# Kernel optimization log

Measured on AMD Instinct MI355X. Metric: run time of the kernel, lower is better.

## Reference

```python
import jax, jax.numpy as jnp
import numpy as np
import math

NUM_HEADS = 8
HEAD_DIM = 16  # hidden_features 128 / 8 heads
SCALE = 1.0 / math.sqrt(HEAD_DIM)


def setup_inputs() -> dict:
    key = jax.random.key(0)
    ks = jax.random.split(key, 9)
    N, E, F = 50000, 640000, 128
    node_h = jax.random.normal(ks[0], (N, F), jnp.float32)
    edge_h = jax.random.normal(ks[1], (E, F), jnp.float32)
    # distances kept strictly positive so distance**lambda (and its grad) is well-defined
    distance = jax.random.uniform(ks[2], (E, 1), jnp.float32, minval=0.1, maxval=1.0)
    src = jax.random.randint(ks[3], (E,), 0, N, jnp.int32)
    dst = jax.random.randint(ks[4], (E,), 0, N, jnp.int32)

    def lin(k):
        kw, kb = jax.random.split(k)
        W = jax.random.normal(kw, (F, F), jnp.float32) / math.sqrt(F)
        b = jax.random.normal(kb, (F,), jnp.float32) * 0.02
        return W, b

    Wq, bq = lin(ks[5])
    Wk, bk = lin(ks[6])
    Wv, bv = lin(ks[7])
    Wo, bo = lin(ks[8])
    lam = jnp.array(1.0, jnp.float32)  # attenuation_lambda (clamp in original is a no-op)
    return dict(node_h=node_h, edge_h=edge_h, distance=distance,
                Wq=Wq, bq=bq, Wk=Wk, bk=bk, Wv=Wv, bv=bv, Wo=Wo, bo=bo,
                lam=lam, src=src, dst=dst)


def _segment_softmax(logits, seg, num):
    # softmax over edges sharing the same destination node (DGL mailbox dim=1)
    m = jax.ops.segment_max(logits, seg, num_segments=num)
    m = jax.lax.stop_gradient(jnp.where(jnp.isfinite(m), m, 0.0))
    e = jnp.exp(logits - m[seg])
    den = jax.ops.segment_sum(e, seg, num_segments=num)
    den = jnp.where(den == 0, 1.0, den)  # guard zero in-degree nodes
    return e / den[seg]


def reference(node_h, edge_h, distance, Wq, bq, Wk, bk, Wv, bv, Wo, bo, lam, src, dst):
    N = node_h.shape[0]
    q = (node_h @ Wq.T + bq).reshape(N, NUM_HEADS, HEAD_DIM)
    k = (edge_h @ Wk.T + bk).reshape(-1, NUM_HEADS, HEAD_DIM)
    v = (node_h @ Wv.T + bv).reshape(N, NUM_HEADS, HEAD_DIM)
    qs, qd = q[src], q[dst]                      # [E, H, d] gathers
    in_m = jnp.sum(qs * k, axis=-1)              # [E, H]
    out_m = jnp.sum(qd * k, axis=-1)             # [E, H]
    diag_m = jnp.sum(qs * qd, axis=-1)           # [E, H]
    att = jnp.power(distance, lam)               # [E, 1] power-law attenuation
    score = (_segment_softmax(in_m * SCALE, dst, N)
             + _segment_softmax(out_m * SCALE, dst, N)
             + _segment_softmax(diag_m * SCALE, dst, N)) * att  # [E, H]
    # message value is edges.dst['v'] (as in the original), scatter-sum to dst
    h = jax.ops.segment_sum(score[..., None] * v[dst], dst, num_segments=N)
    h = h.reshape(N, NUM_HEADS * HEAD_DIM)
    out = h @ Wo.T + bo
    return jax.nn.leaky_relu(out, negative_slope=0.1)  # dropout is identity in eval
```

## Files before the change

kernel.cpp:

```cpp
#include <hip/hip_runtime.h>
#include <math.h>

#define H 8
#define FD 128
#define SCALE 0.25f
#define EPB 128

typedef __attribute__((ext_vector_type(8))) short bf16x8;
typedef __attribute__((ext_vector_type(4))) float f32x4;

__device__ __forceinline__ unsigned short bf_rne(float f) {
    unsigned u = __float_as_uint(f);
    u += 0x7FFFu + ((u >> 16) & 1u);
    return (unsigned short)(u >> 16);
}
__device__ __forceinline__ float bf_to_f(unsigned short s) {
    return __uint_as_float(((unsigned)s) << 16);
}

__global__ __launch_bounds__(256) void edge_kernel(
    const float* __restrict__ eh, const float* __restrict__ Wk,
    const float* __restrict__ bk, const float* __restrict__ q,
    const int* __restrict__ src, const int* __restrict__ dst,
    float* __restrict__ l1, float* __restrict__ l2, float* __restrict__ l3,
    int E) {
    __shared__ unsigned short lW[128 * 128];
    __shared__ unsigned short lA[128 * 128];
    const int t = threadIdx.x;
    const int e0 = blockIdx.x * EPB;

#pragma unroll
    for (int i = 0; i < 16; ++i) {
        int flat = i * 256 + t;
        int row = flat >> 5;
        int c4 = flat & 31;
        float4 w = *(const float4*)(Wk + row * 128 + c4 * 4);
        int blk = (c4 >> 1) ^ (row & 7);
        ushort4 p = make_ushort4(bf_rne(w.x), bf_rne(w.y), bf_rne(w.z), bf_rne(w.w));
        *(ushort4*)(lW + row * 128 + blk * 8 + (c4 & 1) * 4) = p;
    }
#pragma unroll
    for (int i = 0; i < 16; ++i) {
        int flat = i * 256 + t;
        int row = flat >> 5;
        int c4 = flat & 31;
        int e = e0 + row;
        if (e >= E) e = E - 1;
        float4 w = *(const float4*)(eh + (size_t)e * 128 + c4 * 4);
        int blk = (c4 >> 1) ^ (row & 7);
        ushort4 p = make_ushort4(bf_rne(w.x), bf_rne(w.y), bf_rne(w.z), bf_rne(w.w));
        *(ushort4*)(lA + row * 128 + blk * 8 + (c4 & 1) * 4) = p;
    }
    __syncthreads();

    const int lane = t & 63;
    const int wv = t >> 6;
    const int lm = lane & 15;
    const int lq = lane >> 4;
    const int wm = wv * 32;

    bf16x8 a[2][4];
#pragma unroll
    for (int mt = 0; mt < 2; ++mt)
#pragma unroll
        for (int s = 0; s < 4; ++s) {
            int row = wm + mt * 16 + lm;
            int swb = (s * 4 + lq) ^ (row & 7);
            a[mt][s] = *(const bf16x8*)(lA + row * 128 + swb * 8);
        }

    f32x4 acc[2][8];
#pragma unroll
    for (int nt = 0; nt < 8; ++nt) {
        float b = bk[nt * 16 + lm];
#pragma unroll
        for (int mt = 0; mt < 2; ++mt) {
            acc[mt][nt][0] = b; acc[mt][nt][1] = b;
            acc[mt][nt][2] = b; acc[mt][nt][3] = b;
        }
    }
#pragma unroll
    for (int s = 0; s < 4; ++s) {
#pragma unroll
        for (int nt = 0; nt < 8; ++nt) {
            int row = nt * 16 + lm;
            int swb = (s * 4 + lq) ^ (row & 7);
            bf16x8 bf = *(const bf16x8*)(lW + row * 128 + swb * 8);
#pragma unroll
            for (int mt = 0; mt < 2; ++mt)
                acc[mt][nt] = __builtin_amdgcn_mfma_f32_16x16x32_bf16(
                    a[mt][s], bf, acc[mt][nt], 0, 0, 0);
        }
    }
    __syncthreads();
#pragma unroll
    for (int mt = 0; mt < 2; ++mt)
#pragma unroll
        for (int nt = 0; nt < 8; ++nt)
#pragma unroll
            for (int r = 0; r < 4; ++r) {
                int m = wm + mt * 16 + lq * 4 + r;
                int n = nt * 16 + lm;
                int swb = (n >> 3) ^ (m & 7);
                lA[m * 128 + swb * 8 + (n & 7)] = bf_rne(acc[mt][nt][r]);
            }
    __syncthreads();

#pragma unroll
    for (int i = 0; i < 4; ++i) {
        int p = i * 256 + t;
        int el = p >> 3, h = p & 7;
        int e = e0 + el;
        if (e >= E) continue;
        int si = src[e], di = dst[e];
        const float* qsp = q + (size_t)si * FD + h * 16;
        const float* qdp = q + (size_t)di * FD + h * 16;
        float4 s0 = *(const float4*)(qsp);
        float4 s1 = *(const float4*)(qsp + 4);
        float4 s2 = *(const float4*)(qsp + 8);
        float4 s3 = *(const float4*)(qsp + 12);
        float4 d0 = *(const float4*)(qdp);
        float4 d1 = *(const float4*)(qdp + 4);
        float4 d2 = *(const float4*)(qdp + 8);
        float4 d3 = *(const float4*)(qdp + 12);
        int swb0 = (2 * h) ^ (el & 7);
        int swb1 = (2 * h + 1) ^ (el & 7);
        bf16x8 k0 = *(const bf16x8*)(lA + el * 128 + swb0 * 8);
        bf16x8 k1 = *(const bf16x8*)(lA + el * 128 + swb1 * 8);
        float qsv[16] = { s0.x, s0.y, s0.z, s0.w, s1.x, s1.y, s1.z, s1.w,
                          s2.x, s2.y, s2.z, s2.w, s3.x, s3.y, s3.z, s3.w };
        float qdv[16] = { d0.x, d0.y, d0.z, d0.w, d1.x, d1.y, d1.z, d1.w,
                          d2.x, d2.y, d2.z, d2.w, d3.x, d3.y, d3.z, d3.w };
        float pin = 0.f, pot = 0.f, pdg = 0.f;
#pragma unroll
        for (int j = 0; j < 8; ++j) {
            float kf = bf_to_f((unsigned short)k0[j]);
            pin += qsv[j] * kf; pot += qdv[j] * kf; pdg += qsv[j] * qdv[j];
        }
#pragma unroll
        for (int j = 0; j < 8; ++j) {
            float kf = bf_to_f((unsigned short)k1[j]);
            pin += qsv[8 + j] * kf; pot += qdv[8 + j] * kf;
            pdg += qsv[8 + j] * qdv[8 + j];
        }
        size_t gi = (size_t)e * H + h;
        l1[gi] = pin * SCALE;
        l2[gi] = pot * SCALE;
        l3[gi] = pdg * SCALE;
    }
}

__global__ __launch_bounds__(256) void den_kernel(
    float* __restrict__ l1, float* __restrict__ l2, float* __restrict__ l3,
    const int* __restrict__ dst, const float* __restrict__ distance,
    const float* __restrict__ lam, float* __restrict__ den1,
    float* __restrict__ den2, float* __restrict__ den3,
    float* __restrict__ att, int EH) {
    int idx = blockIdx.x * 256 + threadIdx.x;
    if (idx >= EH) return;
    int e = idx >> 3, h = idx & 7;
    int nb = dst[e] * H + h;
    float x1 = __expf(l1[idx]); l1[idx] = x1; atomicAdd(den1 + nb, x1);
    float x2 = __expf(l2[idx]); l2[idx] = x2; atomicAdd(den2 + nb, x2);
    float x3 = __expf(l3[idx]); l3[idx] = x3; atomicAdd(den3 + nb, x3);
    if (h == 0) att[e] = __powf(distance[e], lam[0]);
}

__global__ __launch_bounds__(256) void recip_kernel(
    float* __restrict__ den1, float* __restrict__ den2,
    float* __restrict__ den3, int NH) {
    int idx = blockIdx.x * 256 + threadIdx.x;
    if (idx >= NH) return;
    float d1 = den1[idx]; den1[idx] = (d1 == 0.f) ? 0.f : 1.f / d1;
    float d2 = den2[idx]; den2[idx] = (d2 == 0.f) ? 0.f : 1.f / d2;
    float d3 = den3[idx]; den3[idx] = (d3 == 0.f) ? 0.f : 1.f / d3;
}

__global__ __launch_bounds__(256) void score_kernel(
    const float* __restrict__ l1, const float* __restrict__ l2,
    const float* __restrict__ l3, const float* __restrict__ den1,
    const float* __restrict__ den2, const float* __restrict__ den3,
    const int* __restrict__ dst, const float* __restrict__ att,
    float* __restrict__ ssum, int EH) {
    int idx = blockIdx.x * 256 + threadIdx.x;
    if (idx >= EH) return;
    int e = idx >> 3, h = idx & 7;
    int nb = dst[e] * H + h;
    float sc = (l1[idx] * den1[nb] + l2[idx] * den2[nb] + l3[idx] * den3[nb]) *
               att[e];
    atomicAdd(ssum + nb, sc);
}

__device__ __forceinline__ void load_w_lds(const float* __restrict__ W,
                                           float* Wl, int tid) {
    for (int x = tid; x < (FD * FD) / 4; x += 256) {
        int idx4 = x << 2;
        int i = idx4 >> 7;
        int j = idx4 & 127;
        float4 w = *(const float4*)(W + idx4);
        int col = (j + ((i >> 2) << 2)) & 127;
        *(float4*)(Wl + i * FD + col) = w;
    }
}

__global__ __launch_bounds__(256) void proj_kernel(
    const float* __restrict__ X, const float* __restrict__ W,
    const float* __restrict__ b, float* __restrict__ out, int Nrows) {
    __shared__ float Wl[FD * FD];
    int tid = threadIdx.x;
    load_w_lds(W, Wl, tid);
    __syncthreads();

    int fe = tid & 31;
    int te = tid >> 5;
    int row0 = blockIdx.x * 64;

    float4 bias = *(const float4*)(b + 4 * fe);
    float acc[8][4];
#pragma unroll
    for (int u = 0; u < 8; ++u) {
        acc[u][0] = bias.x; acc[u][1] = bias.y;
        acc[u][2] = bias.z; acc[u][3] = bias.w;
    }
    const float* Ar[8];
#pragma unroll
    for (int u = 0; u < 8; ++u) {
        int r = row0 + te + 8 * u;
        if (r >= Nrows) r = Nrows - 1;
        Ar[u] = X + (size_t)r * FD;
    }
    for (int j = 0; j < FD; j += 4) {
        int g = (j + 4 * fe) & 127;
        float4 w0 = *(float4*)(Wl + (4 * fe + 0) * FD + g);
        float4 w1 = *(float4*)(Wl + (4 * fe + 1) * FD + g);
        float4 w2 = *(float4*)(Wl + (4 * fe + 2) * FD + g);
        float4 w3 = *(float4*)(Wl + (4 * fe + 3) * FD + g);
#pragma unroll
        for (int u = 0; u < 8; ++u) {
            float4 a = *(const float4*)(Ar[u] + j);
            acc[u][0] += a.x * w0.x + a.y * w0.y + a.z * w0.z + a.w * w0.w;
            acc[u][1] += a.x * w1.x + a.y * w1.y + a.z * w1.z + a.w * w1.w;
            acc[u][2] += a.x * w2.x + a.y * w2.y + a.z * w2.z + a.w * w2.w;
            acc[u][3] += a.x * w3.x + a.y * w3.y + a.z * w3.z + a.w * w3.w;
        }
    }
#pragma unroll
    for (int u = 0; u < 8; ++u) {
        int r = row0 + te + 8 * u;
        if (r < Nrows) {
            float4 o;
            o.x = acc[u][0]; o.y = acc[u][1]; o.z = acc[u][2]; o.w = acc[u][3];
            *(float4*)(out + (size_t)r * FD + 4 * fe) = o;
        }
    }
}

__global__ __launch_bounds__(256) void out_kernel(
    const float* __restrict__ v, const float* __restrict__ ssum,
    const float* __restrict__ Wo, const float* __restrict__ bo,
    float* __restrict__ out, int Nrows) {
    __shared__ float Wl[FD * FD];
    int tid = threadIdx.x;
    load_w_lds(Wo, Wl, tid);
    __syncthreads();

    int fe = tid & 31;
    int te = tid >> 5;
    int row0 = blockIdx.x * 64;

    float4 bias = *(const float4*)(bo + 4 * fe);
    float acc[8][4];
#pragma unroll
    for (int u = 0; u < 8; ++u) {
        acc[u][0] = bias.x; acc[u][1] = bias.y;
        acc[u][2] = bias.z; acc[u][3] = bias.w;
    }
    int rv[8];
#pragma unroll
    for (int u = 0; u < 8; ++u) {
        int r = row0 + te + 8 * u;
        rv[u] = (r >= Nrows) ? (Nrows - 1) : r;
    }
    for (int j = 0; j < FD; j += 4) {
        int g = (j + 4 * fe) & 127;
        float4 w0 = *(float4*)(Wl + (4 * fe + 0) * FD + g);
        float4 w1 = *(float4*)(Wl + (4 * fe + 1) * FD + g);
        float4 w2 = *(float4*)(Wl + (4 * fe + 2) * FD + g);
        float4 w3 = *(float4*)(Wl + (4 * fe + 3) * FD + g);
        int hj = j >> 4;
#pragma unroll
        for (int u = 0; u < 8; ++u) {
            float4 a = *(const float4*)(v + (size_t)rv[u] * FD + j);
            float sc = ssum[rv[u] * H + hj];
            a.x *= sc; a.y *= sc; a.z *= sc; a.w *= sc;
            acc[u][0] += a.x * w0.x + a.y * w0.y + a.z * w0.z + a.w * w0.w;
            acc[u][1] += a.x * w1.x + a.y * w1.y + a.z * w1.z + a.w * w1.w;
            acc[u][2] += a.x * w2.x + a.y * w2.y + a.z * w2.z + a.w * w2.w;
            acc[u][3] += a.x * w3.x + a.y * w3.y + a.z * w3.z + a.w * w3.w;
        }
    }
#pragma unroll
    for (int u = 0; u < 8; ++u) {
        int r = row0 + te + 8 * u;
        if (r < Nrows) {
            float4 o;
            o.x = acc[u][0] > 0.f ? acc[u][0] : 0.1f * acc[u][0];
            o.y = acc[u][1] > 0.f ? acc[u][1] : 0.1f * acc[u][1];
            o.z = acc[u][2] > 0.f ? acc[u][2] : 0.1f * acc[u][2];
            o.w = acc[u][3] > 0.f ? acc[u][3] : 0.1f * acc[u][3];
            *(float4*)(out + (size_t)r * FD + 4 * fe) = o;
        }
    }
}

extern "C" void kernel_launch(void* const* d_in, const int* in_sizes, int n_in,
                              void* d_out, int out_size, void* d_ws,
                              size_t ws_size, hipStream_t stream) {
    (void)n_in; (void)out_size; (void)ws_size;
    const float* node_h   = (const float*)d_in[0];
    const float* edge_h   = (const float*)d_in[1];
    const float* distance = (const float*)d_in[2];
    const float* Wq = (const float*)d_in[3];
    const float* bq = (const float*)d_in[4];
    const float* Wk = (const float*)d_in[5];
    const float* bk = (const float*)d_in[6];
    const float* Wv = (const float*)d_in[7];
    const float* bv = (const float*)d_in[8];
    const float* Wo = (const float*)d_in[9];
    const float* bo = (const float*)d_in[10];
    const float* lam = (const float*)d_in[11];
    const int* src = (const int*)d_in[12];
    const int* dst = (const int*)d_in[13];

    int N = in_sizes[0] / FD;
    int E = in_sizes[1] / FD;

    char* ws = (char*)d_ws;
    float* q   = (float*)ws; ws += (size_t)N * FD * 4;
    float* v   = (float*)ws; ws += (size_t)N * FD * 4;
    float* l1  = (float*)ws; ws += (size_t)E * H * 4;
    float* l2  = (float*)ws; ws += (size_t)E * H * 4;
    float* l3  = (float*)ws; ws += (size_t)E * H * 4;
    float* att = (float*)ws; ws += (size_t)E * 4;
    char* zero_base = ws;
    float* den1 = (float*)ws; ws += (size_t)N * H * 4;
    float* den2 = (float*)ws; ws += (size_t)N * H * 4;
    float* den3 = (float*)ws; ws += (size_t)N * H * 4;
    float* ssum = (float*)ws; ws += (size_t)N * H * 4;

    hipMemsetAsync(zero_base, 0, (size_t)4 * N * H * 4, stream);

    int nb = (N + 63) / 64;
    proj_kernel<<<nb, 256, 0, stream>>>(node_h, Wq, bq, q, N);
    proj_kernel<<<nb, 256, 0, stream>>>(node_h, Wv, bv, v, N);

    int ebl = (E + EPB - 1) / EPB;
    edge_kernel<<<ebl, 256, 0, stream>>>(edge_h, Wk, bk, q, src, dst,
                                         l1, l2, l3, E);
    int EH = E * H;
    int sb = (EH + 255) / 256;
    den_kernel<<<sb, 256, 0, stream>>>(l1, l2, l3, dst, distance, lam,
                                       den1, den2, den3, att, EH);
    int NH = N * H;
    recip_kernel<<<(NH + 255) / 256, 256, 0, stream>>>(den1, den2, den3, NH);
    score_kernel<<<sb, 256, 0, stream>>>(l1, l2, l3, den1, den2, den3,
                                         dst, att, ssum, EH);
    out_kernel<<<nb, 256, 0, stream>>>(v, ssum, Wo, bo, (float*)d_out, N);
}
```

Measured before the change: 840.5 us.

## Fuse softmax passes into edge kernel and move projections to bf16 MFMA

Weights are pre-converted to bf16 once, and the Q/V projections are fused into one MFMA kernel that stores q in bf16. The edge kernel now exponentiates the logits directly and atomically accumulates both the softmax denominators and the attenuated numerators per destination node. This removes the E×H logit buffers and the separate den, recip and score passes. A small combine kernel divides the numerators by the denominators, and the output projection also uses bf16 MFMA. Skipping max subtraction in the softmax risks overflow for large logits, bf16 q and v lower precision, and the edge kernel now issues twice as many atomics.

```diff
diff --git a/kernel.cpp b/kernel.cpp
--- a/kernel.cpp
+++ b/kernel.cpp
@@ -4,7 +4,6 @@
 #define H 8
 #define FD 128
 #define SCALE 0.25f
-#define EPB 128
 
 typedef __attribute__((ext_vector_type(8))) short bf16x8;
 typedef __attribute__((ext_vector_type(4))) float f32x4;
@@ -17,58 +16,115 @@
 __device__ __forceinline__ float bf_to_f(unsigned short s) {
     return __uint_as_float(((unsigned)s) << 16);
 }
+__device__ __forceinline__ bf16x8 cvt8(const float* __restrict__ p) {
+    float4 a = *(const float4*)p;
+    float4 b = *(const float4*)(p + 4);
+    bf16x8 r;
+    r[0] = bf_rne(a.x); r[1] = bf_rne(a.y); r[2] = bf_rne(a.z); r[3] = bf_rne(a.w);
+    r[4] = bf_rne(b.x); r[5] = bf_rne(b.y); r[6] = bf_rne(b.z); r[7] = bf_rne(b.w);
+    return r;
+}
+
+__global__ __launch_bounds__(256) void prep_kernel(
+    const float* __restrict__ Wq, const float* __restrict__ Wk,
+    const float* __restrict__ Wv, const float* __restrict__ Wo,
+    unsigned short* __restrict__ oq, unsigned short* __restrict__ ok,
+    unsigned short* __restrict__ ov, unsigned short* __restrict__ oo) {
+    int i = blockIdx.x * 256 + threadIdx.x;
+    const float* src[4] = {Wq, Wk, Wv, Wo};
+    unsigned short* dstp[4] = {oq, ok, ov, oo};
+#pragma unroll
+    for (int m = 0; m < 4; ++m) {
+        float4 w = ((const float4*)src[m])[i];
+        ushort4 p = make_ushort4(bf_rne(w.x), bf_rne(w.y), bf_rne(w.z), bf_rne(w.w));
+        *(ushort4*)(dstp[m] + i * 4) = p;
+    }
+}
+
+__global__ __launch_bounds__(256) void qv_kernel(
+    const float* __restrict__ X, const unsigned short* __restrict__ Wqb,
+    const unsigned short* __restrict__ Wvb, const float* __restrict__ bq,
+    const float* __restrict__ bv, unsigned short* __restrict__ qb,
+    float* __restrict__ v, int Nrows) {
+    const int t = threadIdx.x;
+    const int lane = t & 63, wid = t >> 6;
+    const int lm = lane & 15, lq = lane >> 4;
+    const int r0 = blockIdx.x * 128 + wid * 32;
+
+    bf16x8 a[2][4];
+#pragma unroll
+    for (int mt = 0; mt < 2; ++mt)
+#pragma unroll
+        for (int s = 0; s < 4; ++s) {
+            int r = r0 + mt * 16 + lm;
+            if (r >= Nrows) r = Nrows - 1;
+            a[mt][s] = cvt8(X + (size_t)r * FD + s * 32 + lq * 8);
+        }
+#pragma unroll
+    for (int g = 0; g < 2; ++g) {
+        const unsigned short* Wb = g ? Wvb : Wqb;
+        const float* bias = g ? bv : bq;
+        f32x4 acc[2][8];
+#pragma unroll
+        for (int nt = 0; nt < 8; ++nt) {
+            float b = bias[nt * 16 + lm];
+#pragma unroll
+            for (int mt = 0; mt < 2; ++mt) {
+                acc[mt][nt][0] = b; acc[mt][nt][1] = b;
+                acc[mt][nt][2] = b; acc[mt][nt][3] = b;
+            }
+        }
+#pragma unroll
+        for (int s = 0; s < 4; ++s)
+#pragma unroll
+            for (int nt = 0; nt < 8; ++nt) {
+                bf16x8 bf = *(const bf16x8*)(Wb + (nt * 16 + lm) * FD + s * 32 + lq * 8);
+#pragma unroll
+                for (int mt = 0; mt < 2; ++mt)
+                    acc[mt][nt] = __builtin_amdgcn_mfma_f32_16x16x32_bf16(
+                        a[mt][s], bf, acc[mt][nt], 0, 0, 0);
+            }
+#pragma unroll
+        for (int mt = 0; mt < 2; ++mt)
+#pragma unroll
+            for (int nt = 0; nt < 8; ++nt)
+#pragma unroll
+                for (int r = 0; r < 4; ++r) {
+                    int row = r0 + mt * 16 + lq * 4 + r;
+                    if (row >= Nrows) continue;
+                    int col = nt * 16 + lm;
+                    if (g == 0)
+                        qb[(size_t)row * FD + col] = bf_rne(acc[mt][nt][r]);
+                    else
+                        v[(size_t)row * FD + col] = acc[mt][nt][r];
+                }
+    }
+}
 
 __global__ __launch_bounds__(256) void edge_kernel(
-    const float* __restrict__ eh, const float* __restrict__ Wk,
-    const float* __restrict__ bk, const float* __restrict__ q,
+    const float* __restrict__ eh, const unsigned short* __restrict__ Wkb,
+    const float* __restrict__ bk, const unsigned short* __restrict__ qb,
     const int* __restrict__ src, const int* __restrict__ dst,
-    float* __restrict__ l1, float* __restrict__ l2, float* __restrict__ l3,
-    int E) {
-    __shared__ unsigned short lW[128 * 128];
-    __shared__ unsigned short lA[128 * 128];
+    const float* __restrict__ distance, const float* __restrict__ lam,
+    float* __restrict__ den1, float* __restrict__ den2,
+    float* __restrict__ den3, float* __restrict__ sc1,
+    float* __restrict__ sc2, float* __restrict__ sc3, int E) {
+    __shared__ unsigned short lK[128 * 128];
     const int t = threadIdx.x;
-    const int e0 = blockIdx.x * EPB;
-
-#pragma unroll
-    for (int i = 0; i < 16; ++i) {
-        int flat = i * 256 + t;
-        int row = flat >> 5;
-        int c4 = flat & 31;
-        float4 w = *(const float4*)(Wk + row * 128 + c4 * 4);
-        int blk = (c4 >> 1) ^ (row & 7);
-        ushort4 p = make_ushort4(bf_rne(w.x), bf_rne(w.y), bf_rne(w.z), bf_rne(w.w));
-        *(ushort4*)(lW + row * 128 + blk * 8 + (c4 & 1) * 4) = p;
-    }
-#pragma unroll
-    for (int i = 0; i < 16; ++i) {
-        int flat = i * 256 + t;
-        int row = flat >> 5;
-        int c4 = flat & 31;
-        int e = e0 + row;
-        if (e >= E) e = E - 1;
-        float4 w = *(const float4*)(eh + (size_t)e * 128 + c4 * 4);
-        int blk = (c4 >> 1) ^ (row & 7);
-        ushort4 p = make_ushort4(bf_rne(w.x), bf_rne(w.y), bf_rne(w.z), bf_rne(w.w));
-        *(ushort4*)(lA + row * 128 + blk * 8 + (c4 & 1) * 4) = p;
-    }
-    __syncthreads();
-
-    const int lane = t & 63;
-    const int wv = t >> 6;
-    const int lm = lane & 15;
-    const int lq = lane >> 4;
-    const int wm = wv * 32;
+    const int e0 = blockIdx.x * 128;
+    const int lane = t & 63, wid = t >> 6;
+    const int lm = lane & 15, lq = lane >> 4;
+    const int wm = wid * 32;
 
     bf16x8 a[2][4];
 #pragma unroll
     for (int mt = 0; mt < 2; ++mt)
 #pragma unroll
         for (int s = 0; s < 4; ++s) {
-            int row = wm + mt * 16 + lm;
-            int swb = (s * 4 + lq) ^ (row & 7);
-            a[mt][s] = *(const bf16x8*)(lA + row * 128 + swb * 8);
-        }
-
+            int e = e0 + wm + mt * 16 + lm;
+            if (e >= E) e = E - 1;
+            a[mt][s] = cvt8(eh + (size_t)e * FD + s * 32 + lq * 8);
+        }
     f32x4 acc[2][8];
 #pragma unroll
     for (int nt = 0; nt < 8; ++nt) {
@@ -80,19 +136,15 @@
         }
     }
 #pragma unroll
-    for (int s = 0; s < 4; ++s) {
+    for (int s = 0; s < 4; ++s)
 #pragma unroll
         for (int nt = 0; nt < 8; ++nt) {
-            int row = nt * 16 + lm;
-            int swb = (s * 4 + lq) ^ (row & 7);
-            bf16x8 bf = *(const bf16x8*)(lW + row * 128 + swb * 8);
+            bf16x8 bf = *(const bf16x8*)(Wkb + (nt * 16 + lm) * FD + s * 32 + lq * 8);
 #pragma unroll
             for (int mt = 0; mt < 2; ++mt)
                 acc[mt][nt] = __builtin_amdgcn_mfma_f32_16x16x32_bf16(
                     a[mt][s], bf, acc[mt][nt], 0, 0, 0);
         }
-    }
-    __syncthreads();
 #pragma unroll
     for (int mt = 0; mt < 2; ++mt)
 #pragma unroll
@@ -102,10 +154,11 @@
                 int m = wm + mt * 16 + lq * 4 + r;
                 int n = nt * 16 + lm;
                 int swb = (n >> 3) ^ (m & 7);
-                lA[m * 128 + swb * 8 + (n & 7)] = bf_rne(acc[mt][nt][r]);
+                lK[m * 128 + swb * 8 + (n & 7)] = bf_rne(acc[mt][nt][r]);
             }
     __syncthreads();
 
+    const float lamv = lam[0];
 #pragma unroll
     for (int i = 0; i < 4; ++i) {
         int p = i * 256 + t;
@@ -113,204 +166,115 @@
         int e = e0 + el;
         if (e >= E) continue;
         int si = src[e], di = dst[e];
-        const float* qsp = q + (size_t)si * FD + h * 16;
-        const float* qdp = q + (size_t)di * FD + h * 16;
-        float4 s0 = *(const float4*)(qsp);
-        float4 s1 = *(const float4*)(qsp + 4);
-        float4 s2 = *(const float4*)(qsp + 8);
-        float4 s3 = *(const float4*)(qsp + 12);
-        float4 d0 = *(const float4*)(qdp);
-        float4 d1 = *(const float4*)(qdp + 4);
-        float4 d2 = *(const float4*)(qdp + 8);
-        float4 d3 = *(const float4*)(qdp + 12);
-        int swb0 = (2 * h) ^ (el & 7);
-        int swb1 = (2 * h + 1) ^ (el & 7);
-        bf16x8 k0 = *(const bf16x8*)(lA + el * 128 + swb0 * 8);
-        bf16x8 k1 = *(const bf16x8*)(lA + el * 128 + swb1 * 8);
-        float qsv[16] = { s0.x, s0.y, s0.z, s0.w, s1.x, s1.y, s1.z, s1.w,
-                          s2.x, s2.y, s2.z, s2.w, s3.x, s3.y, s3.z, s3.w };
-        float qdv[16] = { d0.x, d0.y, d0.z, d0.w, d1.x, d1.y, d1.z, d1.w,
-                          d2.x, d2.y, d2.z, d2.w, d3.x, d3.y, d3.z, d3.w };
+        const unsigned short* qsp = qb + (size_t)si * FD + h * 16;
+        const unsigned short* qdp = qb + (size_t)di * FD + h * 16;
+        bf16x8 qs0 = *(const bf16x8*)qsp;
+        bf16x8 qs1 = *(const bf16x8*)(qsp + 8);
+        bf16x8 qd0 = *(const bf16x8*)qdp;
+        bf16x8 qd1 = *(const bf16x8*)(qdp + 8);
+        int swb0 = (2 * h) ^ (el & 7), swb1 = (2 * h + 1) ^ (el & 7);
+        bf16x8 k0 = *(const bf16x8*)(lK + el * 128 + swb0 * 8);
+        bf16x8 k1 = *(const bf16x8*)(lK + el * 128 + swb1 * 8);
         float pin = 0.f, pot = 0.f, pdg = 0.f;
 #pragma unroll
         for (int j = 0; j < 8; ++j) {
+            float qsf = bf_to_f((unsigned short)qs0[j]);
+            float qdf = bf_to_f((unsigned short)qd0[j]);
             float kf = bf_to_f((unsigned short)k0[j]);
-            pin += qsv[j] * kf; pot += qdv[j] * kf; pdg += qsv[j] * qdv[j];
+            pin += qsf * kf; pot += qdf * kf; pdg += qsf * qdf;
         }
 #pragma unroll
         for (int j = 0; j < 8; ++j) {
+            float qsf = bf_to_f((unsigned short)qs1[j]);
+            float qdf = bf_to_f((unsigned short)qd1[j]);
             float kf = bf_to_f((unsigned short)k1[j]);
-            pin += qsv[8 + j] * kf; pot += qdv[8 + j] * kf;
-            pdg += qsv[8 + j] * qdv[8 + j];
-        }
-        size_t gi = (size_t)e * H + h;
-        l1[gi] = pin * SCALE;
-        l2[gi] = pot * SCALE;
-        l3[gi] = pdg * SCALE;
-    }
-}
-
-__global__ __launch_bounds__(256) void den_kernel(
-    float* __restrict__ l1, float* __restrict__ l2, float* __restrict__ l3,
-    const int* __restrict__ dst, const float* __restrict__ distance,
-    const float* __restrict__ lam, float* __restrict__ den1,
-    float* __restrict__ den2, float* __restrict__ den3,
-    float* __restrict__ att, int EH) {
-    int idx = blockIdx.x * 256 + threadIdx.x;
-    if (idx >= EH) return;
-    int e = idx >> 3, h = idx & 7;
-    int nb = dst[e] * H + h;
-    float x1 = __expf(l1[idx]); l1[idx] = x1; atomicAdd(den1 + nb, x1);
-    float x2 = __expf(l2[idx]); l2[idx] = x2; atomicAdd(den2 + nb, x2);
-    float x3 = __expf(l3[idx]); l3[idx] = x3; atomicAdd(den3 + nb, x3);
-    if (h == 0) att[e] = __powf(distance[e], lam[0]);
-}
-
-__global__ __launch_bounds__(256) void recip_kernel(
-    float* __restrict__ den1, float* __restrict__ den2,
-    float* __restrict__ den3, int NH) {
-    int idx = blockIdx.x * 256 + threadIdx.x;
-    if (idx >= NH) return;
-    float d1 = den1[idx]; den1[idx] = (d1 == 0.f) ? 0.f : 1.f / d1;
-    float d2 = den2[idx]; den2[idx] = (d2 == 0.f) ? 0.f : 1.f / d2;
-    float d3 = den3[idx]; den3[idx] = (d3 == 0.f) ? 0.f : 1.f / d3;
-}
-
-__global__ __launch_bounds__(256) void score_kernel(
-    const float* __restrict__ l1, const float* __restrict__ l2,
-    const float* __restrict__ l3, const float* __restrict__ den1,
-    const float* __restrict__ den2, const float* __restrict__ den3,
-    const int* __restrict__ dst, const float* __restrict__ att,
-    float* __restrict__ ssum, int EH) {
-    int idx = blockIdx.x * 256 + threadIdx.x;
-    if (idx >= EH) return;
-    int e = idx >> 3, h = idx & 7;
-    int nb = dst[e] * H + h;
-    float sc = (l1[idx] * den1[nb] + l2[idx] * den2[nb] + l3[idx] * den3[nb]) *
-               att[e];
-    atomicAdd(ssum + nb, sc);
-}
-
-__device__ __forceinline__ void load_w_lds(const float* __restrict__ W,
-                                           float* Wl, int tid) {
-    for (int x = tid; x < (FD * FD) / 4; x += 256) {
-        int idx4 = x << 2;
-        int i = idx4 >> 7;
-        int j = idx4 & 127;
-        float4 w = *(const float4*)(W + idx4);
-        int col = (j + ((i >> 2) << 2)) & 127;
-        *(float4*)(Wl + i * FD + col) = w;
-    }
-}
-
-__global__ __launch_bounds__(256) void proj_kernel(
-    const float* __restrict__ X, const float* __restrict__ W,
-    const float* __restrict__ b, float* __restrict__ out, int Nrows) {
-    __shared__ float Wl[FD * FD];
-    int tid = threadIdx.x;
-    load_w_lds(W, Wl, tid);
-    __syncthreads();
-
-    int fe = tid & 31;
-    int te = tid >> 5;
-    int row0 = blockIdx.x * 64;
-
-    float4 bias = *(const float4*)(b + 4 * fe);
-    float acc[8][4];
-#pragma unroll
-    for (int u = 0; u < 8; ++u) {
-        acc[u][0] = bias.x; acc[u][1] = bias.y;
-        acc[u][2] = bias.z; acc[u][3] = bias.w;
-    }
-    const float* Ar[8];
-#pragma unroll
-    for (int u = 0; u < 8; ++u) {
-        int r = row0 + te + 8 * u;
-        if (r >= Nrows) r = Nrows - 1;
-        Ar[u] = X + (size_t)r * FD;
-    }
-    for (int j = 0; j < FD; j += 4) {
-        int g = (j + 4 * fe) & 127;
-        float4 w0 = *(float4*)(Wl + (4 * fe + 0) * FD + g);
-        float4 w1 = *(float4*)(Wl + (4 * fe + 1) * FD + g);
-        float4 w2 = *(float4*)(Wl + (4 * fe + 2) * FD + g);
-        float4 w3 = *(float4*)(Wl + (4 * fe + 3) * FD + g);
-#pragma unroll
-        for (int u = 0; u < 8; ++u) {
-            float4 a = *(const float4*)(Ar[u] + j);
-            acc[u][0] += a.x * w0.x + a.y * w0.y + a.z * w0.z + a.w * w0.w;
-            acc[u][1] += a.x * w1.x + a.y * w1.y + a.z * w1.z + a.w * w1.w;
-            acc[u][2] += a.x * w2.x + a.y * w2.y + a.z * w2.z + a.w * w2.w;
-            acc[u][3] += a.x * w3.x + a.y * w3.y + a.z * w3.z + a.w * w3.w;
-        }
-    }
-#pragma unroll
-    for (int u = 0; u < 8; ++u) {
-        int r = row0 + te + 8 * u;
-        if (r < Nrows) {
-            float4 o;
-            o.x = acc[u][0]; o.y = acc[u][1]; o.z = acc[u][2]; o.w = acc[u][3];
-            *(float4*)(out + (size_t)r * FD + 4 * fe) = o;
-        }
-    }
+            pin += qsf * kf; pot += qdf * kf; pdg += qsf * qdf;
+        }
+        float att = __expf(lamv * __logf(distance[e]));
+        float e1 = __expf(pin * SCALE);
+        float e2 = __expf(pot * SCALE);
+        float e3 = __expf(pdg * SCALE);
+        int nb = di * H + h;
+        atomicAdd(den1 + nb, e1); atomicAdd(sc1 + nb, e1 * att);
+        atomicAdd(den2 + nb, e2); atomicAdd(sc2 + nb, e2 * att);
+        atomicAdd(den3 + nb, e3); atomicAdd(sc3 + nb, e3 * att);
+    }
+}
+
+__global__ __launch_bounds__(256) void combine_kernel(
+    const float* __restrict__ den1, const float* __restrict__ den2,
+    const float* __restrict__ den3, const float* __restrict__ sc1,
+    const float* __restrict__ sc2, const float* __restrict__ sc3,
+    float* __restrict__ ssum, int NH) {
+    int i = blockIdx.x * 256 + threadIdx.x;
+    if (i >= NH) return;
+    float r = 0.f;
+    float d1 = den1[i]; if (d1 != 0.f) r += sc1[i] / d1;
+    float d2 = den2[i]; if (d2 != 0.f) r += sc2[i] / d2;
+    float d3 = den3[i]; if (d3 != 0.f) r += sc3[i] / d3;
+    ssum[i] = r;
 }
 
 __global__ __launch_bounds__(256) void out_kernel(
     const float* __restrict__ v, const float* __restrict__ ssum,
-    const float* __restrict__ Wo, const float* __restrict__ bo,
+    const unsigned short* __restrict__ Wob, const float* __restrict__ bo,
     float* __restrict__ out, int Nrows) {
-    __shared__ float Wl[FD * FD];
-    int tid = threadIdx.x;
-    load_w_lds(Wo, Wl, tid);
-    __syncthreads();
-
-    int fe = tid & 31;
-    int te = tid >> 5;
-    int row0 = blockIdx.x * 64;
-
-    float4 bias = *(const float4*)(bo + 4 * fe);
-    float acc[8][4];
-#pragma unroll
-    for (int u = 0; u < 8; ++u) {
-        acc[u][0] = bias.x; acc[u][1] = bias.y;
-        acc[u][2] = bias.z; acc[u][3] = bias.w;
-    }
-    int rv[8];
-#pragma unroll
-    for (int u = 0; u < 8; ++u) {
-        int r = row0 + te + 8 * u;
-        rv[u] = (r >= Nrows) ? (Nrows - 1) : r;
-    }
-    for (int j = 0; j < FD; j += 4) {
-        int g = (j + 4 * fe) & 127;
-        float4 w0 = *(float4*)(Wl + (4 * fe + 0) * FD + g);
-        float4 w1 = *(float4*)(Wl + (4 * fe + 1) * FD + g);
-        float4 w2 = *(float4*)(Wl + (4 * fe + 2) * FD + g);
-        float4 w3 = *(float4*)(Wl + (4 * fe + 3) * FD + g);
-        int hj = j >> 4;
-#pragma unroll
-        for (int u = 0; u < 8; ++u) {
-            float4 a = *(const float4*)(v + (size_t)rv[u] * FD + j);
-            float sc = ssum[rv[u] * H + hj];
-            a.x *= sc; a.y *= sc; a.z *= sc; a.w *= sc;
-            acc[u][0] += a.x * w0.x + a.y * w0.y + a.z * w0.z + a.w * w0.w;
-            acc[u][1] += a.x * w1.x + a.y * w1.y + a.z * w1.z + a.w * w1.w;
-            acc[u][2] += a.x * w2.x + a.y * w2.y + a.z * w2.z + a.w * w2.w;
-            acc[u][3] += a.x * w3.x + a.y * w3.y + a.z * w3.z + a.w * w3.w;
-        }
-    }
-#pragma unroll
-    for (int u = 0; u < 8; ++u) {
-        int r = row0 + te + 8 * u;
-        if (r < Nrows) {
-            float4 o;
-            o.x = acc[u][0] > 0.f ? acc[u][0] : 0.1f * acc[u][0];
-            o.y = acc[u][1] > 0.f ? acc[u][1] : 0.1f * acc[u][1];
-            o.z = acc[u][2] > 0.f ? acc[u][2] : 0.1f * acc[u][2];
-            o.w = acc[u][3] > 0.f ? acc[u][3] : 0.1f * acc[u][3];
-            *(float4*)(out + (size_t)r * FD + 4 * fe) = o;
-        }
-    }
+    const int t = threadIdx.x;
+    const int lane = t & 63, wid = t >> 6;
+    const int lm = lane & 15, lq = lane >> 4;
+    const int r0 = blockIdx.x * 128 + wid * 32;
+
+    bf16x8 a[2][4];
+#pragma unroll
+    for (int mt = 0; mt < 2; ++mt)
+#pragma unroll
+        for (int s = 0; s < 4; ++s) {
+            int r = r0 + mt * 16 + lm;
+            if (r >= Nrows) r = Nrows - 1;
+            int k0 = s * 32 + lq * 8;
+            float sc = ssum[r * H + (k0 >> 4)];
+            const float* p = v + (size_t)r * FD + k0;
+            float4 x = *(const float4*)p;
+            float4 y = *(const float4*)(p + 4);
+            bf16x8 f;
+            f[0] = bf_rne(x.x * sc); f[1] = bf_rne(x.y * sc);
+            f[2] = bf_rne(x.z * sc); f[3] = bf_rne(x.w * sc);
+            f[4] = bf_rne(y.x * sc); f[5] = bf_rne(y.y * sc);
+            f[6] = bf_rne(y.z * sc); f[7] = bf_rne(y.w * sc);
+            a[mt][s] = f;
+        }
+    f32x4 acc[2][8];
+#pragma unroll
+    for (int nt = 0; nt < 8; ++nt) {
+        float b = bo[nt * 16 + lm];
+#pragma unroll
+        for (int mt = 0; mt < 2; ++mt) {
+            acc[mt][nt][0] = b; acc[mt][nt][1] = b;
+            acc[mt][nt][2] = b; acc[mt][nt][3] = b;
+        }
+    }
+#pragma unroll
+    for (int s = 0; s < 4; ++s)
+#pragma unroll
+        for (int nt = 0; nt < 8; ++nt) {
+            bf16x8 bf = *(const bf16x8*)(Wob + (nt * 16 + lm) * FD + s * 32 + lq * 8);
+#pragma unroll
+            for (int mt = 0; mt < 2; ++mt)
+                acc[mt][nt] = __builtin_amdgcn_mfma_f32_16x16x32_bf16(
+                    a[mt][s], bf, acc[mt][nt], 0, 0, 0);
+        }
+#pragma unroll
+    for (int mt = 0; mt < 2; ++mt)
+#pragma unroll
+        for (int nt = 0; nt < 8; ++nt)
+#pragma unroll
+            for (int r = 0; r < 4; ++r) {
+                int row = r0 + mt * 16 + lq * 4 + r;
+                if (row >= Nrows) continue;
+                int col = nt * 16 + lm;
+                float x = acc[mt][nt][r];
+                out[(size_t)row * FD + col] = x > 0.f ? x : 0.1f * x;
+            }
 }
 
 extern "C" void kernel_launch(void* const* d_in, const int* in_sizes, int n_in,
@@ -334,36 +298,38 @@
 
     int N = in_sizes[0] / FD;
     int E = in_sizes[1] / FD;
+    int NH = N * H;
 
     char* ws = (char*)d_ws;
-    float* q   = (float*)ws; ws += (size_t)N * FD * 4;
-    float* v   = (float*)ws; ws += (size_t)N * FD * 4;
-    float* l1  = (float*)ws; ws += (size_t)E * H * 4;
-    float* l2  = (float*)ws; ws += (size_t)E * H * 4;
-    float* l3  = (float*)ws; ws += (size_t)E * H * 4;
-    float* att = (float*)ws; ws += (size_t)E * 4;
+    unsigned short* Wqb = (unsigned short*)ws; ws += FD * FD * 2;
+    unsigned short* Wkb = (unsigned short*)ws; ws += FD * FD * 2;
+    unsigned short* Wvb = (unsigned short*)ws; ws += FD * FD * 2;
+    unsigned short* Wob = (unsigned short*)ws; ws += FD * FD * 2;
+    unsigned short* qb  = (unsigned short*)ws; ws += (size_t)N * FD * 2;
+    float* v    = (float*)ws; ws += (size_t)N * FD * 4;
     char* zero_base = ws;
-    float* den1 = (float*)ws; ws += (size_t)N * H * 4;
-    float* den2 = (float*)ws; ws += (size_t)N * H * 4;
-    float* den3 = (float*)ws; ws += (size_t)N * H * 4;
-    float* ssum = (float*)ws; ws += (size_t)N * H * 4;
-
-    hipMemsetAsync(zero_base, 0, (size_t)4 * N * H * 4, stream);
-
-    int nb = (N + 63) / 64;
-    proj_kernel<<<nb, 256, 0, stream>>>(node_h, Wq, bq, q, N);
-    proj_kernel<<<nb, 256, 0, stream>>>(node_h, Wv, bv, v, N);
-
-    int ebl = (E + EPB - 1) / EPB;
-    edge_kernel<<<ebl, 256, 0, stream>>>(edge_h, Wk, bk, q, src, dst,
-                                         l1, l2, l3, E);
-    int EH = E * H;
-    int sb = (EH + 255) / 256;
-    den_kernel<<<sb, 256, 0, stream>>>(l1, l2, l3, dst, distance, lam,
-                                       den1, den2, den3, att, EH);
-    int NH = N * H;
-    recip_kernel<<<(NH + 255) / 256, 256, 0, stream>>>(den1, den2, den3, NH);
-    score_kernel<<<sb, 256, 0, stream>>>(l1, l2, l3, den1, den2, den3,
-                                         dst, att, ssum, EH);
-    out_kernel<<<nb, 256, 0, stream>>>(v, ssum, Wo, bo, (float*)d_out, N);
-}
+    float* den1 = (float*)ws; ws += (size_t)NH * 4;
+    float* den2 = (float*)ws; ws += (size_t)NH * 4;
+    float* den3 = (float*)ws; ws += (size_t)NH * 4;
+    float* sc1  = (float*)ws; ws += (size_t)NH * 4;
+    float* sc2  = (float*)ws; ws += (size_t)NH * 4;
+    float* sc3  = (float*)ws; ws += (size_t)NH * 4;
+    float* ssum = (float*)ws; ws += (size_t)NH * 4;
+
+    hipMemsetAsync(zero_base, 0, (size_t)6 * NH * 4, stream);
+
+    prep_kernel<<<16, 256, 0, stream>>>(Wq, Wk, Wv, Wo, Wqb, Wkb, Wvb, Wob);
+
+    int nb = (N + 127) / 128;
+    qv_kernel<<<nb, 256, 0, stream>>>(node_h, Wqb, Wvb, bq, bv, qb, v, N);
+
+    int ebl = (E + 127) / 128;
+    edge_kernel<<<ebl, 256, 0, stream>>>(edge_h, Wkb, bk, qb, src, dst,
+                                         distance, lam,
+                                         den1, den2, den3, sc1, sc2, sc3, E);
+
+    combine_kernel<<<(NH + 255) / 256, 256, 0, stream>>>(
+        den1, den2, den3, sc1, sc2, sc3, ssum, NH);
+
+    out_kernel<<<nb, 256, 0, stream>>>(v, ssum, Wob, bo, (float*)d_out, N);
+}
```

After: 676.4 us. 19.5% less time.
